# Performance work log

Hardware: AMD Instinct MI355X
Metric: run time of the kernel (lower is better)

The kernel has to match this reference:

```python
import jax, jax.numpy as jnp
import numpy as np

NUM_HEADS = 8
GRAPH_DIM = 64
K_RATIO = 0.1
SIM_THRESH = 0.6


def _gat_layer(h_in, mask, W, a_src, a_dst, b):
    # PyG GATConv (heads=1, eval mode): lin (no bias), alpha = LeakyReLU(a_src.h_j + a_dst.h_i),
    # softmax over source nodes j per target i (edges given by dense mask, self loops included), + bias.
    h = h_in @ W                                   # [N, F]
    asrc = h @ a_src                               # [N] source term
    adst = h @ a_dst                               # [N] target term
    logits = jax.nn.leaky_relu(adst[:, None] + asrc[None, :], 0.2)  # [target i, source j]
    logits = jnp.where(mask.T, logits, -1e30)      # mask[j,i]: edge src j -> dst i (symmetric here)
    alpha = jax.nn.softmax(logits, axis=-1)
    return alpha @ h + b


def _forward(x, w_qkv, w_proj, b_proj, gat0_W, gat0_asrc, gat0_adst, gat0_b,
             gat1_W, gat1_asrc, gat1_adst, gat1_b, w_g2a, b_g2a):
    B, C, H, W = x.shape
    HW = H * W
    nh = NUM_HEADS
    hd = C // nh
    scale = hd ** -0.5
    x_seq = x.reshape(B, C, HW).transpose(0, 2, 1)                 # [B, HW, C]

    # ---- build_spatial_graph ----
    importance = jnp.var(x_seq, axis=-1, ddof=1)                   # torch.var default unbiased
    N = int(HW * K_RATIO)                                          # 102 nodes
    _, top_idx = jax.lax.top_k(importance, N)                      # [B, N]
    feats = jnp.take_along_axis(x_seq, top_idx[..., None], axis=1) # [B, N, C]
    fn = feats / jnp.clip(jnp.linalg.norm(feats, axis=-1, keepdims=True), 1e-12)
    sim = fn @ fn.transpose(0, 2, 1)                               # [B, N, N]
    adj = sim > SIM_THRESH
    adj = adj | jnp.eye(N, dtype=bool)                             # GATConv add_self_loops

    # ---- per-batch GAT stack + graph_to_attn ----
    def per_graph(f, m):
        g = jax.nn.relu(_gat_layer(f, m, gat0_W, gat0_asrc, gat0_adst, gat0_b))
        g = jax.nn.relu(_gat_layer(g, m, gat1_W, gat1_asrc, gat1_adst, gat1_b))
        return jax.nn.sigmoid(g @ w_g2a.T + b_g2a)                 # [N, nh]
    gw = jax.vmap(per_graph)(feats, adj)                           # [B, N, nh]

    # ---- dense multi-head attention ----
    qkv = (x_seq @ w_qkv.T).reshape(B, HW, 3, nh, hd).transpose(2, 0, 3, 1, 4)
    q, k, v = qkv[0], qkv[1], qkv[2]                               # [B, nh, HW, hd]
    scores = jnp.einsum('bhqd,bhkd->bhqk', q, k) * scale           # [B, nh, HW, HW]

    # ---- graph modulation scatter (replaces the nested python loops) ----
    vals = jnp.where(adj[..., None], gw[:, :, None, :] * gw[:, None, :, :], 0.0)  # [B, N, N, nh]
    gm = jnp.zeros_like(scores)
    bidx = jnp.arange(B)[:, None, None]
    gm = gm.at[bidx, :, top_idx[:, :, None], top_idx[:, None, :]].set(vals)
    scores = scores + gm

    attn = jax.nn.softmax(scores, axis=-1)                         # dropout is identity in eval
    out = jnp.einsum('bhqk,bhkd->bhqd', attn, v).transpose(0, 2, 1, 3).reshape(B, HW, C)
    out = out @ w_proj.T + b_proj
    return out.transpose(0, 2, 1).reshape(B, C, H, W)


def setup_inputs() -> dict:
    key = jax.random.key(0)
    ks = jax.random.split(key, 16)
    dim, gd, nh = 256, GRAPH_DIM, NUM_HEADS
    B, H, W = 8, 32, 32
    s = 0.02
    return {
        'x': jax.random.normal(ks[0], (B, dim, H, W), dtype=jnp.float32),
        'w_qkv': s * jax.random.normal(ks[1], (3 * dim, dim), dtype=jnp.float32),
        'w_proj': s * jax.random.normal(ks[2], (dim, dim), dtype=jnp.float32),
        'b_proj': jnp.zeros((dim,), dtype=jnp.float32),
        'gat0_W': s * jax.random.normal(ks[3], (dim, gd), dtype=jnp.float32),
        'gat0_asrc': s * jax.random.normal(ks[4], (gd,), dtype=jnp.float32),
        'gat0_adst': s * jax.random.normal(ks[5], (gd,), dtype=jnp.float32),
        'gat0_b': jnp.zeros((gd,), dtype=jnp.float32),
        'gat1_W': s * jax.random.normal(ks[6], (gd, gd), dtype=jnp.float32),
        'gat1_asrc': s * jax.random.normal(ks[7], (gd,), dtype=jnp.float32),
        'gat1_adst': s * jax.random.normal(ks[8], (gd,), dtype=jnp.float32),
        'gat1_b': jnp.zeros((gd,), dtype=jnp.float32),
        'w_g2a': s * jax.random.normal(ks[9], (nh, gd), dtype=jnp.float32),
        'b_g2a': jnp.zeros((nh,), dtype=jnp.float32),
    }


def reference(x, w_qkv, w_proj, b_proj, gat0_W, gat0_asrc, gat0_adst, gat0_b,
              gat1_W, gat1_asrc, gat1_adst, gat1_b, w_g2a, b_g2a):
    return _forward(x, w_qkv, w_proj, b_proj, gat0_W, gat0_asrc, gat0_adst, gat0_b,
                    gat1_W, gat1_asrc, gat1_adst, gat1_b, w_g2a, b_g2a)
```

## Files before the change

kernel.cpp:

```cpp
#include <hip/hip_runtime.h>
#include <math.h>

#define NB 8
#define CDIM 256
#define HWD 1024
#define NH 8
#define HD 32
#define NN 102
#define GD 64

typedef __attribute__((ext_vector_type(8))) short bf16x8;
typedef __attribute__((ext_vector_type(4))) float f32x4;

__device__ inline short f2bf(float f) {
  union { float f; unsigned u; } v; v.f = f;
  unsigned r = v.u + 0x7fffu + ((v.u >> 16) & 1u);
  return (short)(r >> 16);
}
__device__ inline float bf2f(short s) {
  union { unsigned u; float f; } v;
  v.u = ((unsigned)(unsigned short)s) << 16;
  return v.f;
}

__global__ __launch_bounds__(256) void wsplit_k(const float* __restrict__ w_qkv,
                                                const float* __restrict__ w_proj,
                                                short* __restrict__ wqh, short* __restrict__ wql,
                                                short* __restrict__ wph, short* __restrict__ wpl) {
  int t = blockIdx.x * 256 + threadIdx.x;
  if (t < 196608) {
    float v = w_qkv[t];
    short hi = f2bf(v);
    wqh[t] = hi; wql[t] = f2bf(v - bf2f(hi));
  } else {
    int u = t - 196608;
    float v = w_proj[u];
    short hi = f2bf(v);
    wph[u] = hi; wpl[u] = f2bf(v - bf2f(hi));
  }
}

__global__ __launch_bounds__(256) void xsplit_k(const float* __restrict__ x,
                                                short* __restrict__ xth,
                                                short* __restrict__ xtl) {
  __shared__ float tile[64][65];
  int p0 = blockIdx.x * 64, c0 = blockIdx.y * 64, b = blockIdx.z;
  int t = threadIdx.x;
  {
    int g = t >> 6, p = t & 63;
#pragma unroll
    for (int i = 0; i < 16; ++i) {
      int cc = g * 16 + i;
      tile[cc][p] = x[((size_t)(b * 256 + c0 + cc)) * 1024 + p0 + p];
    }
  }
  __syncthreads();
  {
    int p = t >> 2, cs = (t & 3) * 16;
    size_t rb = ((size_t)(b * 1024 + p0 + p)) * 256 + c0 + cs;
#pragma unroll
    for (int g = 0; g < 4; ++g) {
      short4 hv, lv;
      float f0 = tile[cs + g * 4 + 0][p];
      float f1 = tile[cs + g * 4 + 1][p];
      float f2 = tile[cs + g * 4 + 2][p];
      float f3 = tile[cs + g * 4 + 3][p];
      hv.x = f2bf(f0); lv.x = f2bf(f0 - bf2f(hv.x));
      hv.y = f2bf(f1); lv.y = f2bf(f1 - bf2f(hv.y));
      hv.z = f2bf(f2); lv.z = f2bf(f2 - bf2f(hv.z));
      hv.w = f2bf(f3); lv.w = f2bf(f3 - bf2f(hv.w));
      *(short4*)(xth + rb + g * 4) = hv;
      *(short4*)(xtl + rb + g * 4) = lv;
    }
  }
}

__global__ __launch_bounds__(256) void prep_k(const float* __restrict__ g0W,
                                              const float* __restrict__ g1W,
                                              short* __restrict__ w0bT,
                                              short* __restrict__ w1bT) {
  int t = blockIdx.x * 256 + threadIdx.x;
  if (t < 16384) {
    int c = t >> 6, f = t & 63;
    w0bT[f * 256 + c] = f2bf(g0W[t]);
  } else if (t < 20480) {
    int u2 = t - 16384;
    int c = u2 >> 6, f = u2 & 63;
    w1bT[f * 64 + c] = f2bf(g1W[u2]);
  }
}

__global__ __launch_bounds__(256) void importance_k(const float* __restrict__ x,
                                                    float* __restrict__ imp) {
  __shared__ float red[8][33];
  int bp = blockIdx.x;
  int b = bp >> 5, p0 = (bp & 31) << 5;
  int t = threadIdx.x;
  int pl = t & 31, cg = t >> 5;
  const float* xp = x + (size_t)b * CDIM * HWD + p0 + pl;
  float s = 0.f;
  for (int cc = 0; cc < 32; ++cc) s += xp[(size_t)(cg * 32 + cc) * HWD];
  red[cg][pl] = s;
  __syncthreads();
  float tot = 0.f;
  for (int g = 0; g < 8; ++g) tot += red[g][pl];
  float mean = tot * (1.f / CDIM);
  __syncthreads();
  float v = 0.f;
  for (int cc = 0; cc < 32; ++cc) {
    float d = xp[(size_t)(cg * 32 + cc) * HWD] - mean;
    v += d * d;
  }
  red[cg][pl] = v;
  __syncthreads();
  if (t < 32) {
    float vv = 0.f;
    for (int g = 0; g < 8; ++g) vv += red[g][t];
    imp[b * 1024 + p0 + t] = vv * (1.f / (CDIM - 1));
  }
}

union GraphLDS {
  struct { float sv[1024]; int si[1024]; } tk;
  struct {
    short h0T[64 * 136];
    short alphaB[102 * 136];
    short gB[102 * 72];
  } m;
};

__global__ __launch_bounds__(1024) void graph_k(
    const float* __restrict__ x, const float* __restrict__ imp,
    const short* __restrict__ w0bT, const short* __restrict__ w1bT,
    const float* __restrict__ g0as, const float* __restrict__ g0ad,
    const float* __restrict__ g0b,
    const float* __restrict__ g1as, const float* __restrict__ g1ad,
    const float* __restrict__ g1b,
    const float* __restrict__ wg2a, const float* __restrict__ bg2a,
    int* __restrict__ nodeof, int* __restrict__ topi, short* __restrict__ fnG,
    unsigned char* __restrict__ adjG, float* __restrict__ gwb) {
  __shared__ GraphLDS u;
  __shared__ ushort adjPack[NN][8];
  __shared__ float normL[NN];
  __shared__ float asrcL[NN], adstL[NN];
  __shared__ int topiL[NN];
  int b = blockIdx.x, t = threadIdx.x;
  int wv = t >> 6, lane = t & 63, quad = lane >> 4, l16 = lane & 15;

  u.tk.sv[t] = imp[b * 1024 + t];
  u.tk.si[t] = t;
  nodeof[b * 1024 + t] = -1;
  __syncthreads();
  for (int k = 2; k <= 1024; k <<= 1) {
    for (int j = k >> 1; j > 0; j >>= 1) {
      int ixj = t ^ j;
      if (ixj > t) {
        bool up = ((t & k) == 0);
        float a = u.tk.sv[t], c = u.tk.sv[ixj];
        if ((a > c) == up) {
          u.tk.sv[t] = c; u.tk.sv[ixj] = a;
          int ti = u.tk.si[t]; u.tk.si[t] = u.tk.si[ixj]; u.tk.si[ixj] = ti;
        }
      }
      __syncthreads();
    }
  }
  if (t >= 1024 - NN) {
    int n = 1023 - t;
    int idx = u.tk.si[t];
    topiL[n] = idx;
    topi[b * 128 + n] = idx;
    nodeof[b * 1024 + idx] = n;
  }
  __syncthreads();

  {
    int n = t >> 3, g = t & 7;
    if (n < NN) {
      int idx = topiL[n];
      const float* xb = x + (size_t)b * CDIM * HWD + idx;
      float vbuf[32];
      float ssl = 0.f;
#pragma unroll
      for (int cc = 0; cc < 32; ++cc) {
        float v = xb[(size_t)(g * 32 + cc) * HWD];
        vbuf[cc] = v;
        ssl += v * v;
      }
      ssl += __shfl_xor(ssl, 1);
      ssl += __shfl_xor(ssl, 2);
      ssl += __shfl_xor(ssl, 4);
      float nrm = sqrtf(ssl);
      float rn = 1.f / fmaxf(nrm, 1e-12f);
      if (g == 0) normL[n] = nrm;
      short* fp = fnG + ((size_t)b * 112 + n) * 256 + g * 32;
#pragma unroll
      for (int cc = 0; cc < 32; cc += 4) {
        short4 s4 = {f2bf(vbuf[cc] * rn), f2bf(vbuf[cc + 1] * rn),
                     f2bf(vbuf[cc + 2] * rn), f2bf(vbuf[cc + 3] * rn)};
        *(short4*)(fp + cc) = s4;
      }
    }
  }
  for (int e = t; e < 64 * 34; e += 1024) {
    int f = e / 34, c = 102 + (e % 34);
    u.m.h0T[f * 136 + c] = 0;
  }
  __syncthreads();

  for (int tile = wv; tile < 49; tile += 16) {
    int I = tile / 7, J = tile % 7;
    const short* ap = fnG + ((size_t)b * 112 + I * 16 + l16) * 256 + quad * 8;
    const short* bp = fnG + ((size_t)b * 112 + J * 16 + l16) * 256 + quad * 8;
    f32x4 acc = (f32x4){0.f, 0.f, 0.f, 0.f};
#pragma unroll
    for (int kb = 0; kb < 8; ++kb)
      acc = __builtin_amdgcn_mfma_f32_16x16x32_bf16(*(const bf16x8*)(ap + kb * 32),
                                                    *(const bf16x8*)(bp + kb * 32), acc, 0, 0, 0);
#pragma unroll
    for (int r = 0; r < 4; ++r) {
      int i = I * 16 + quad * 4 + r, j = J * 16 + l16;
      bool e = (acc[r] > 0.6f) || (i == j);
      unsigned long long m = __ballot(e);
      if (l16 == 0) {
        int row = I * 16 + quad * 4 + r;
        if (row < NN) adjPack[row][J] = (ushort)((m >> (quad * 16)) & 0xFFFFull);
      }
      if (i < NN && j < NN) adjG[(size_t)b * NN * NN + i * NN + j] = e ? 1 : 0;
    }
  }
  __syncthreads();

  for (int tile = wv; tile < 28; tile += 16) {
    int mt = tile >> 2, nt = tile & 3;
    const short* ap = fnG + ((size_t)b * 112 + mt * 16 + l16) * 256 + quad * 8;
    const short* bp = w0bT + (nt * 16 + l16) * 256 + quad * 8;
    f32x4 acc = (f32x4){0.f, 0.f, 0.f, 0.f};
#pragma unroll
    for (int kb = 0; kb < 8; ++kb)
      acc = __builtin_amdgcn_mfma_f32_16x16x32_bf16(*(const bf16x8*)(ap + kb * 32),
                                                    *(const bf16x8*)(bp + kb * 32), acc, 0, 0, 0);
    int f = nt * 16 + l16;
#pragma unroll
    for (int r = 0; r < 4; ++r) {
      int node = mt * 16 + quad * 4 + r;
      if (node < NN) u.m.h0T[f * 136 + node] = f2bf(acc[r] * normL[node]);
    }
  }
  __syncthreads();

  for (int layer = 0; layer < 2; ++layer) {
    const float* avs = layer ? g1as : g0as;
    const float* avd = layer ? g1ad : g0ad;
    const float* bias = layer ? g1b : g0b;
    {
      int n = t >> 3, g = t & 7;
      if (n < NN) {
        float s1 = 0.f, s2 = 0.f;
#pragma unroll
        for (int uu = 0; uu < 8; ++uu) {
          int f = g * 8 + uu;
          float hv = bf2f(u.m.h0T[f * 136 + n]);
          s1 += hv * avs[f];
          s2 += hv * avd[f];
        }
        s1 += __shfl_xor(s1, 1); s1 += __shfl_xor(s1, 2); s1 += __shfl_xor(s1, 4);
        s2 += __shfl_xor(s2, 1); s2 += __shfl_xor(s2, 2); s2 += __shfl_xor(s2, 4);
        if (g == 0) { asrcL[n] = s1; adstL[n] = s2; }
      }
    }
    __syncthreads();
    for (int i = wv; i < NN; i += 16) {
      float zi = adstL[i];
      int j1 = 64 + lane;
      bool e0 = (adjPack[i][lane >> 4] >> (lane & 15)) & 1;
      bool e1 = (j1 < NN) && ((adjPack[i][j1 >> 4] >> (j1 & 15)) & 1);
      float p0 = 0.f, p1 = 0.f;
      if (e0) { float z = zi + asrcL[lane]; p0 = __expf(z > 0.f ? z : 0.2f * z); }
      if (e1) { float z = zi + asrcL[j1]; p1 = __expf(z > 0.f ? z : 0.2f * z); }
      float s = p0 + p1;
      s += __shfl_xor(s, 1); s += __shfl_xor(s, 2); s += __shfl_xor(s, 4);
      s += __shfl_xor(s, 8); s += __shfl_xor(s, 16); s += __shfl_xor(s, 32);
      float inv = 1.f / s;
      u.m.alphaB[i * 136 + lane] = f2bf(p0 * inv);
      u.m.alphaB[i * 136 + 64 + lane] = f2bf(p1 * inv);
    }
    __syncthreads();
    for (int tile = wv; tile < 28; tile += 16) {
      int mt = tile >> 2, nt = tile & 3;
      int ar = mt * 16 + l16; if (ar > NN - 1) ar = NN - 1;
      const short* ap = &u.m.alphaB[ar * 136 + quad * 8];
      const short* bp = &u.m.h0T[(nt * 16 + l16) * 136 + quad * 8];
      f32x4 acc = (f32x4){0.f, 0.f, 0.f, 0.f};
#pragma unroll
      for (int kb = 0; kb < 4; ++kb)
        acc = __builtin_amdgcn_mfma_f32_16x16x32_bf16(*(const bf16x8*)(ap + kb * 32),
                                                      *(const bf16x8*)(bp + kb * 32), acc, 0, 0, 0);
      int f = nt * 16 + l16;
      float bv = bias[f];
#pragma unroll
      for (int r = 0; r < 4; ++r) {
        int i = mt * 16 + quad * 4 + r;
        if (i < NN) u.m.gB[i * 72 + f] = f2bf(fmaxf(acc[r] + bv, 0.f));
      }
    }
    __syncthreads();
    if (layer == 0) {
      for (int tile = wv; tile < 28; tile += 16) {
        int mt = tile >> 2, nt = tile & 3;
        int ar = mt * 16 + l16; if (ar > NN - 1) ar = NN - 1;
        const short* ap = &u.m.gB[ar * 72 + quad * 8];
        const short* bp = w1bT + (nt * 16 + l16) * 64 + quad * 8;
        f32x4 acc = (f32x4){0.f, 0.f, 0.f, 0.f};
#pragma unroll
        for (int kb = 0; kb < 2; ++kb)
          acc = __builtin_amdgcn_mfma_f32_16x16x32_bf16(*(const bf16x8*)(ap + kb * 32),
                                                        *(const bf16x8*)(bp + kb * 32), acc, 0, 0, 0);
        int f = nt * 16 + l16;
#pragma unroll
        for (int r = 0; r < 4; ++r) {
          int node = mt * 16 + quad * 4 + r;
          if (node < NN) u.m.h0T[f * 136 + node] = f2bf(acc[r]);
        }
      }
      __syncthreads();
    }
  }
  float* wgL = (float*)&u.m.alphaB[0];
  if (t < 512) wgL[t] = wg2a[t];
  __syncthreads();
  if (t < NN * NH) {
    int n = t >> 3, h = t & 7;
    float z = bg2a[h];
#pragma unroll
    for (int c = 0; c < GD; ++c) z += bf2f(u.m.gB[n * 72 + c]) * wgL[h * 64 + c];
    gwb[((size_t)b * NN + n) * NH + h] = 1.f / (1.f + __expf(-z));
  }
}

__global__ __launch_bounds__(128) void posadj_k(const int* __restrict__ nodeof,
                                                const int* __restrict__ topi,
                                                const unsigned char* __restrict__ adjG,
                                                const float* __restrict__ gwb,
                                                unsigned long long* __restrict__ posadj,
                                                float* __restrict__ gwp) {
  int b = blockIdx.y, p = blockIdx.x * 128 + threadIdx.x;
  int n = nodeof[b * 1024 + p];
#pragma unroll
  for (int h = 0; h < 8; ++h)
    gwp[(size_t)(b * 8 + h) * 1024 + p] =
        (n >= 0) ? gwb[((size_t)b * NN + n) * NH + h] : 0.f;
  unsigned long long m[16];
#pragma unroll
  for (int w = 0; w < 16; ++w) m[w] = 0;
  if (n >= 0) {
    const unsigned char* ar = adjG + (size_t)b * NN * NN + (size_t)n * NN;
    for (int nj = 0; nj < NN; ++nj) {
      if (ar[nj]) {
        int pj = topi[b * 128 + nj];
        m[pj >> 6] |= 1ull << (pj & 63);
      }
    }
  }
  unsigned long long* dst = posadj + (size_t)(b * 1024 + p) * 16;
#pragma unroll
  for (int w = 0; w < 16; ++w) dst[w] = m[w];
}

__global__ __launch_bounds__(256, 4) void qkv_k(const short* __restrict__ xth,
                                                const short* __restrict__ xtl,
                                                const short* __restrict__ wqh,
                                                const short* __restrict__ wql,
                                                short* __restrict__ qhp, short* __restrict__ qlp,
                                                short* __restrict__ khp, short* __restrict__ klp,
                                                short* __restrict__ vtp) {
  __shared__ short vs_s[4][32 * 24];
  int t = threadIdx.x, wid = t >> 6, lane = t & 63, quad = lane >> 4, l16 = lane & 15;
  int m0 = blockIdx.x * 64, y = blockIdx.y;
  int b = m0 >> 10;
  int row = m0 + wid * 16 + l16;
  int p_base = (m0 & 1023) + wid * 16;
  int qi = y >> 3, n0 = (y & 7) * 32;
  const short* wh = wqh + ((size_t)qi * 256 + n0) * 256;
  const short* wl = wql + ((size_t)qi * 256 + n0) * 256;
  const short* arh = xth + (size_t)row * 256 + quad * 8;
  const short* arl = xtl + (size_t)row * 256 + quad * 8;
  f32x4 acc[2];
  acc[0] = (f32x4){0.f, 0.f, 0.f, 0.f};
  acc[1] = (f32x4){0.f, 0.f, 0.f, 0.f};
#pragma unroll
  for (int kb = 0; kb < 8; ++kb) {
    bf16x8 ah = *(const bf16x8*)(arh + kb * 32);
    bf16x8 al = *(const bf16x8*)(arl + kb * 32);
#pragma unroll
    for (int nt = 0; nt < 2; ++nt) {
      size_t wo = (size_t)(nt * 16 + l16) * 256 + kb * 32 + quad * 8;
      bf16x8 bh_ = *(const bf16x8*)(wh + wo);
      bf16x8 bl_ = *(const bf16x8*)(wl + wo);
      acc[nt] = __builtin_amdgcn_mfma_f32_16x16x32_bf16(ah, bh_, acc[nt], 0, 0, 0);
      acc[nt] = __builtin_amdgcn_mfma_f32_16x16x32_bf16(ah, bl_, acc[nt], 0, 0, 0);
      acc[nt] = __builtin_amdgcn_mfma_f32_16x16x32_bf16(al, bh_, acc[nt], 0, 0, 0);
    }
  }
  if (qi < 2) {
    const float scale = (qi == 0) ? 0.17677669529663687f : 1.f;
    short* hp = (qi == 0) ? qhp : khp;
    short* lp = (qi == 0) ? qlp : klp;
#pragma unroll
    for (int nt = 0; nt < 2; ++nt) {
      int nq = n0 + nt * 16 + l16;
      int h = nq >> 5, d = nq & 31;
#pragma unroll
      for (int r = 0; r < 4; ++r) {
        int p = p_base + quad * 4 + r;
        float v = acc[nt][r] * scale;
        short hi = f2bf(v);
        short lo = f2bf(v - bf2f(hi));
        size_t e = ((size_t)(b * 8 + h) * 1024 + p) * 32 + d;
        hp[e] = hi;
        lp[e] = lo;
      }
    }
  } else {
    short* vs = &vs_s[wid][0];
#pragma unroll
    for (int nt = 0; nt < 2; ++nt)
#pragma unroll
      for (int r = 0; r < 4; ++r)
        vs[(nt * 16 + l16) * 24 + quad * 4 + r] = f2bf(acc[nt][r]);
    int cl = lane >> 1, hf = lane & 1;
    int nq = n0 + cl;
    int h = nq >> 5, d = nq & 31;
    size_t rb = ((size_t)(b * 8 + h) * 32 + d) * 1024 + p_base + hf * 8;
    *(bf16x8*)(vtp + rb) = *(const bf16x8*)(vs + cl * 24 + hf * 8);
  }
}

__global__ __launch_bounds__(256, 4) void attn_k(const short* __restrict__ qh,
                                                 const short* __restrict__ ql,
                                                 const short* __restrict__ kh,
                                                 const short* __restrict__ kl,
                                                 const short* __restrict__ vt,
                                                 const float* __restrict__ gwp,
                                                 const unsigned long long* __restrict__ posadj,
                                                 float* __restrict__ po,
                                                 float* __restrict__ pl) {
  __shared__ __align__(16) short p_s[4][16 * 72];
  __shared__ float aw_s[4][16];
  int t = threadIdx.x;
  int wid = t >> 6, lane = t & 63, quad = lane >> 4, l16 = lane & 15;
  int bh = blockIdx.x, b = bh >> 3;
  int qt = blockIdx.y, khalf = blockIdx.z;
  int q0 = qt * 64 + wid * 16;
  size_t base = (size_t)bh * 32768;
  short* pw = &p_s[wid][0];
  float* aw = &aw_s[wid][0];

  size_t qoff = base + (size_t)(q0 + l16) * 32 + quad * 8;
  bf16x8 qhf = *(const bf16x8*)(qh + qoff);
  bf16x8 qlf = *(const bf16x8*)(ql + qoff);

  const float* gwpBH = gwp + (size_t)bh * 1024;
  const unsigned long long* paB = posadj + (size_t)b * 1024 * 16;
  float grq[4];
#pragma unroll
  for (int r = 0; r < 4; ++r) grq[r] = gwpBH[q0 + quad * 4 + r];

  f32x4 ot[2];
  ot[0] = (f32x4){0.f, 0.f, 0.f, 0.f};
  ot[1] = (f32x4){0.f, 0.f, 0.f, 0.f};
  float l_r[4] = {0.f, 0.f, 0.f, 0.f};

  for (int ch = khalf * 8; ch < khalf * 8 + 8; ++ch) {
    int c0 = ch * 64;
    bf16x8 khf[4], klf[4];
#pragma unroll
    for (int ni = 0; ni < 4; ++ni) {
      size_t off = base + (size_t)(c0 + ni * 16 + l16) * 32 + quad * 8;
      khf[ni] = *(const bf16x8*)(kh + off);
      klf[ni] = *(const bf16x8*)(kl + off);
    }
    bf16x8 vaf[2][2];
#pragma unroll
    for (int mi = 0; mi < 2; ++mi)
#pragma unroll
      for (int ks = 0; ks < 2; ++ks)
        vaf[mi][ks] = *(const bf16x8*)(vt + base + (size_t)(mi * 16 + l16) * 1024 +
                                       c0 + ks * 32 + quad * 8);
    float gc[4];
#pragma unroll
    for (int ni = 0; ni < 4; ++ni) gc[ni] = gwpBH[c0 + ni * 16 + l16];
    unsigned long long mr[4];
#pragma unroll
    for (int r = 0; r < 4; ++r)
      mr[r] = paB[(size_t)(q0 + quad * 4 + r) * 16 + ch];
    f32x4 s[4];
#pragma unroll
    for (int ni = 0; ni < 4; ++ni) {
      f32x4 a = (f32x4){0.f, 0.f, 0.f, 0.f};
      a = __builtin_amdgcn_mfma_f32_16x16x32_bf16(qhf, khf[ni], a, 0, 0, 0);
      a = __builtin_amdgcn_mfma_f32_16x16x32_bf16(qhf, klf[ni], a, 0, 0, 0);
      a = __builtin_amdgcn_mfma_f32_16x16x32_bf16(qlf, khf[ni], a, 0, 0, 0);
      s[ni] = a;
    }
#pragma unroll
    for (int r = 0; r < 4; ++r) {
#pragma unroll
      for (int ni = 0; ni < 4; ++ni) {
        bool bit = (mr[r] >> (ni * 16 + l16)) & 1ull;
        s[ni][r] += bit ? grq[r] * gc[ni] : 0.f;
      }
    }
#pragma unroll
    for (int r = 0; r < 4; ++r) {
      float e0 = __expf(s[0][r]);
      float e1 = __expf(s[1][r]);
      float e2 = __expf(s[2][r]);
      float e3 = __expf(s[3][r]);
      l_r[r] += (e0 + e1) + (e2 + e3);
      int prow = (quad * 4 + r) * 72;
      pw[prow + 0 + l16] = f2bf(e0);
      pw[prow + 16 + l16] = f2bf(e1);
      pw[prow + 32 + l16] = f2bf(e2);
      pw[prow + 48 + l16] = f2bf(e3);
    }
#pragma unroll
    for (int ks = 0; ks < 2; ++ks) {
      bf16x8 pb = *(const bf16x8*)(pw + l16 * 72 + ks * 32 + quad * 8);
      ot[0] = __builtin_amdgcn_mfma_f32_16x16x32_bf16(vaf[0][ks], pb, ot[0], 0, 0, 0);
      ot[1] = __builtin_amdgcn_mfma_f32_16x16x32_bf16(vaf[1][ks], pb, ot[1], 0, 0, 0);
    }
  }
#pragma unroll
  for (int r = 0; r < 4; ++r) {
    float ls = l_r[r];
    ls += __shfl_xor(ls, 1);
    ls += __shfl_xor(ls, 2);
    ls += __shfl_xor(ls, 4);
    ls += __shfl_xor(ls, 8);
    if (l16 == 0) aw[quad * 4 + r] = ls;
  }
  float* os = (float*)pw;
#pragma unroll
  for (int mi = 0; mi < 2; ++mi)
#pragma unroll
    for (int r = 0; r < 4; ++r)
      os[l16 * 36 + mi * 16 + quad * 4 + r] = ot[mi][r];
  int bht = bh * 16 + qt;
  size_t pob = (((size_t)bht * 2 + khalf) * 64 + wid * 16) * 32;
  int qr2 = lane >> 2, dg = (lane & 3) * 8;
  *(float4*)&po[pob + qr2 * 32 + dg] = *(float4*)&os[qr2 * 36 + dg];
  *(float4*)&po[pob + qr2 * 32 + dg + 4] = *(float4*)&os[qr2 * 36 + dg + 4];
  if (lane < 16) pl[((size_t)bht * 2 + khalf) * 64 + wid * 16 + lane] = aw[lane];
}

__global__ __launch_bounds__(256) void reduce_k(const float* __restrict__ po,
                                                const float* __restrict__ pl,
                                                short* __restrict__ aoh,
                                                short* __restrict__ aol) {
  int bht = blockIdx.x;
  int bh = bht >> 4, qt = bht & 15;
  int b = bh >> 3, h = bh & 7;
  int t = threadIdx.x;
  int q = t >> 2, dg = (t & 3) * 8;
  size_t b0 = (((size_t)bht * 2 + 0) * 64 + q) * 32 + dg;
  size_t b1 = (((size_t)bht * 2 + 1) * 64 + q) * 32 + dg;
  float4 a0 = *(const float4*)&po[b0];
  float4 a1 = *(const float4*)&po[b0 + 4];
  float4 c0 = *(const float4*)&po[b1];
  float4 c1 = *(const float4*)&po[b1 + 4];
  float l = pl[((size_t)bht * 2) * 64 + q] + pl[((size_t)bht * 2 + 1) * 64 + q];
  float inv = 1.f / l;
  float f[8] = {(a0.x + c0.x) * inv, (a0.y + c0.y) * inv,
                (a0.z + c0.z) * inv, (a0.w + c0.w) * inv,
                (a1.x + c1.x) * inv, (a1.y + c1.y) * inv,
                (a1.z + c1.z) * inv, (a1.w + c1.w) * inv};
  bf16x8 hv, lv;
#pragma unroll
  for (int j = 0; j < 8; ++j) {
    hv[j] = f2bf(f[j]);
    lv[j] = f2bf(f[j] - bf2f(hv[j]));
  }
  size_t ob = (size_t)(b * 1024 + qt * 64 + q) * 256 + h * 32 + dg;
  *(bf16x8*)(aoh + ob) = hv;
  *(bf16x8*)(aol + ob) = lv;
}

__global__ __launch_bounds__(256, 4) void proj_k(const short* __restrict__ aoh,
                                                 const short* __restrict__ aol,
                                                 const short* __restrict__ wph,
                                                 const short* __restrict__ wpl,
                                                 const float* __restrict__ bias,
                                                 float* __restrict__ out) {
  __shared__ float os_s[4][32 * 20];
  int t = threadIdx.x, wid = t >> 6, lane = t & 63, quad = lane >> 4, l16 = lane & 15;
  int m0 = blockIdx.x * 64, n0 = blockIdx.y * 32;
  int b = m0 >> 10;
  int row = m0 + wid * 16 + l16;
  int p_base = (m0 & 1023) + wid * 16;
  const short* arh = aoh + (size_t)row * 256 + quad * 8;
  const short* arl = aol + (size_t)row * 256 + quad * 8;
  f32x4 acc[2];
  acc[0] = (f32x4){0.f, 0.f, 0.f, 0.f};
  acc[1] = (f32x4){0.f, 0.f, 0.f, 0.f};
#pragma unroll
  for (int kb = 0; kb < 8; ++kb) {
// ... 27 lines not shown
extern "C" void kernel_launch(void* const* d_in, const int* in_sizes, int n_in,
                              void* d_out, int out_size, void* d_ws, size_t ws_size,
                              hipStream_t stream) {
  const float* x      = (const float*)d_in[0];
  const float* w_qkv  = (const float*)d_in[1];
  const float* w_proj = (const float*)d_in[2];
  const float* b_proj = (const float*)d_in[3];
  const float* g0W    = (const float*)d_in[4];
  const float* g0as   = (const float*)d_in[5];
  const float* g0ad   = (const float*)d_in[6];
  const float* g0b    = (const float*)d_in[7];
  const float* g1W    = (const float*)d_in[8];
  const float* g1as   = (const float*)d_in[9];
  const float* g1ad   = (const float*)d_in[10];
  const float* g1b    = (const float*)d_in[11];
  const float* wg2a   = (const float*)d_in[12];
  const float* bg2a   = (const float*)d_in[13];
  float* out = (float*)d_out;
  float* ws = (float*)d_ws;

  size_t o = 0;
  auto alloc = [&](size_t nf) { float* p = ws + o; o += (nf + 15) & ~(size_t)15; return p; };
  float* imp    = alloc(8 * 1024);
  int*   nodeof = (int*)alloc(8 * 1024);
  int*   topi   = (int*)alloc(8 * 128);
  short* fnG    = (short*)alloc(8 * 112 * 256 / 2);
  short* w0bT   = (short*)alloc(256 * 64 / 2);
  short* w1bT   = (short*)alloc(64 * 64 / 2);
  unsigned char* adj = (unsigned char*)alloc((8 * NN * NN + 3) / 4 + 16);
  float* gwb    = alloc(8 * NN * 8);
  unsigned long long* posadj = (unsigned long long*)alloc(8 * 1024 * 16 * 2);
  float* gwp    = alloc(64 * 1024);
  short* xth    = (short*)alloc(1048576);
  short* xtl    = (short*)alloc(1048576);
  short* wqh    = (short*)alloc(98304);
  short* wql    = (short*)alloc(98304);
  short* wph    = (short*)alloc(32768);
  short* wpl    = (short*)alloc(32768);
  short* qh     = (short*)alloc(1048576);
  short* ql     = (short*)alloc(1048576);
  short* kh     = (short*)alloc(1048576);
  short* kl     = (short*)alloc(1048576);
  short* vt     = (short*)alloc(1048576);
  short* aoh    = (short*)alloc(1048576);
  short* aol    = (short*)alloc(1048576);
  float* po     = alloc((size_t)1024 * 2 * 64 * 32);
  float* plv    = alloc((size_t)1024 * 2 * 64);
  if (ws_size < o * sizeof(float)) return;

  importance_k<<<256, 256, 0, stream>>>(x, imp);
  wsplit_k<<<1024, 256, 0, stream>>>(w_qkv, w_proj, wqh, wql, wph, wpl);
  xsplit_k<<<dim3(16, 4, 8), 256, 0, stream>>>(x, xth, xtl);
  prep_k<<<80, 256, 0, stream>>>(g0W, g1W, w0bT, w1bT);
  graph_k<<<8, 1024, 0, stream>>>(x, imp, w0bT, w1bT, g0as, g0ad, g0b,
                                  g1as, g1ad, g1b, wg2a, bg2a,
                                  nodeof, topi, fnG, adj, gwb);
  posadj_k<<<dim3(8, 8), 128, 0, stream>>>(nodeof, topi, adj, gwb, posadj, gwp);
  qkv_k<<<dim3(128, 24), 256, 0, stream>>>(xth, xtl, wqh, wql, qh, ql, kh, kl, vt);
  attn_k<<<dim3(64, 16, 2), 256, 0, stream>>>(qh, ql, kh, kl, vt, gwp, posadj, po, plv);
  reduce_k<<<1024, 256, 0, stream>>>(po, plv, aoh, aol);
  proj_k<<<dim3(128, 8), 256, 0, stream>>>(aoh, aol, wph, wpl, b_proj, out);
}
```

Measured before the change: 365.8 us.

## Fuse prep, posadj and split-K reduce kernels; restructure graph and attention stages

Merges the GAT weight prep into the weight-split kernel, folds posadj construction into graph_k using LDS adjacency bits, and removes the attention split-K plus reduce kernel by having each attention block process all 16 key chunks and normalize in place. graph_k now reads pre-split bf16 transposed x instead of strided fp32 x, applies the norm scaling after the similarity MFMA, and computes the attention-logit dot products inside the linear-layer MFMA epilogue. The posadj layout is transposed to chunk-major, and the qkv store paths are restaged through LDS for wider writes. This cuts kernel launches and intermediate global traffic, but the attention grid is halved (1024 blocks instead of 2048), which lowers parallelism, and graph_k still runs on only 8 blocks.

Result: faster. 300.9 us (-17.7%).

```diff
diff --git a/kernel.cpp b/kernel.cpp
--- a/kernel.cpp
+++ b/kernel.cpp
@@ -23,20 +23,37 @@
   return v.f;
 }
 
-__global__ __launch_bounds__(256) void wsplit_k(const float* __restrict__ w_qkv,
-                                                const float* __restrict__ w_proj,
-                                                short* __restrict__ wqh, short* __restrict__ wql,
-                                                short* __restrict__ wph, short* __restrict__ wpl) {
-  int t = blockIdx.x * 256 + threadIdx.x;
-  if (t < 196608) {
-    float v = w_qkv[t];
-    short hi = f2bf(v);
-    wqh[t] = hi; wql[t] = f2bf(v - bf2f(hi));
+__global__ __launch_bounds__(256) void wsplitprep_k(const float* __restrict__ w_qkv,
+                                                    const float* __restrict__ w_proj,
+                                                    const float* __restrict__ g0W,
+                                                    const float* __restrict__ g1W,
+                                                    short* __restrict__ wqh, short* __restrict__ wql,
+                                                    short* __restrict__ wph, short* __restrict__ wpl,
+                                                    short* __restrict__ w0bT,
+                                                    short* __restrict__ w1bT) {
+  int bx = blockIdx.x;
+  if (bx < 1024) {
+    int t = bx * 256 + threadIdx.x;
+    if (t < 196608) {
+      float v = w_qkv[t];
+      short hi = f2bf(v);
+      wqh[t] = hi; wql[t] = f2bf(v - bf2f(hi));
+    } else {
+      int u = t - 196608;
+      float v = w_proj[u];
+      short hi = f2bf(v);
+      wph[u] = hi; wpl[u] = f2bf(v - bf2f(hi));
+    }
   } else {
-    int u = t - 196608;
-    float v = w_proj[u];
-    short hi = f2bf(v);
-    wph[u] = hi; wpl[u] = f2bf(v - bf2f(hi));
+    int t = (bx - 1024) * 256 + threadIdx.x;
+    if (t < 16384) {
+      int c = t >> 6, f = t & 63;
+      w0bT[f * 256 + c] = f2bf(g0W[t]);
+    } else if (t < 20480) {
+      int u2 = t - 16384;
+      int c = u2 >> 6, f = u2 & 63;
+      w1bT[f * 64 + c] = f2bf(g1W[u2]);
+    }
   }
 }
 
@@ -75,21 +92,6 @@
   }
 }
 
-__global__ __launch_bounds__(256) void prep_k(const float* __restrict__ g0W,
-                                              const float* __restrict__ g1W,
-                                              short* __restrict__ w0bT,
-                                              short* __restrict__ w1bT) {
-  int t = blockIdx.x * 256 + threadIdx.x;
-  if (t < 16384) {
-    int c = t >> 6, f = t & 63;
-    w0bT[f * 256 + c] = f2bf(g0W[t]);
-  } else if (t < 20480) {
-    int u2 = t - 16384;
-    int c = u2 >> 6, f = u2 & 63;
-    w1bT[f * 64 + c] = f2bf(g1W[u2]);
-  }
-}
-
 __global__ __launch_bounds__(256) void importance_k(const float* __restrict__ x,
                                                     float* __restrict__ imp) {
   __shared__ float red[8][33];
@@ -122,34 +124,37 @@
 
 union GraphLDS {
   struct { float sv[1024]; int si[1024]; } tk;
-  struct {
-    short h0T[64 * 136];
-    short alphaB[102 * 136];
-    short gB[102 * 72];
-  } m;
+  short featsB[NN * 264];
+  struct { short alphaB[NN * 136]; short gB[NN * 72]; } ly;
 };
 
 __global__ __launch_bounds__(1024) void graph_k(
-    const float* __restrict__ x, const float* __restrict__ imp,
+    const float* __restrict__ imp,
+    const short* __restrict__ xth, const short* __restrict__ xtl,
     const short* __restrict__ w0bT, const short* __restrict__ w1bT,
     const float* __restrict__ g0as, const float* __restrict__ g0ad,
     const float* __restrict__ g0b,
     const float* __restrict__ g1as, const float* __restrict__ g1ad,
     const float* __restrict__ g1b,
     const float* __restrict__ wg2a, const float* __restrict__ bg2a,
-    int* __restrict__ nodeof, int* __restrict__ topi, short* __restrict__ fnG,
-    unsigned char* __restrict__ adjG, float* __restrict__ gwb) {
+    short* __restrict__ h0tG,
+    float* __restrict__ gwp,
+    unsigned long long* __restrict__ posadj)
+{
   __shared__ GraphLDS u;
   __shared__ ushort adjPack[NN][8];
-  __shared__ float normL[NN];
-  __shared__ float asrcL[NN], adstL[NN];
+  __shared__ float rnL[NN];
+  __shared__ float asrcL[112], adstL[112];
   __shared__ int topiL[NN];
+  __shared__ int nodeofL[1024];
   int b = blockIdx.x, t = threadIdx.x;
   int wv = t >> 6, lane = t & 63, quad = lane >> 4, l16 = lane & 15;
+  short* hb = h0tG + (size_t)b * 64 * 128;
 
   u.tk.sv[t] = imp[b * 1024 + t];
   u.tk.si[t] = t;
-  nodeof[b * 1024 + t] = -1;
+  nodeofL[t] = -1;
+  for (int e = t; e < 64 * 26; e += 1024) hb[(e / 26) * 128 + 102 + (e % 26)] = 0;
   __syncthreads();
   for (int k = 2; k <= 1024; k <<= 1) {
     for (int j = k >> 1; j > 0; j >>= 1) {
@@ -169,49 +174,42 @@
     int n = 1023 - t;
     int idx = u.tk.si[t];
     topiL[n] = idx;
-    topi[b * 128 + n] = idx;
-    nodeof[b * 1024 + idx] = n;
+    nodeofL[idx] = n;
   }
   __syncthreads();
 
   {
     int n = t >> 3, g = t & 7;
     if (n < NN) {
-      int idx = topiL[n];
-      const float* xb = x + (size_t)b * CDIM * HWD + idx;
-      float vbuf[32];
-      float ssl = 0.f;
-#pragma unroll
-      for (int cc = 0; cc < 32; ++cc) {
-        float v = xb[(size_t)(g * 32 + cc) * HWD];
-        vbuf[cc] = v;
-        ssl += v * v;
-      }
-      ssl += __shfl_xor(ssl, 1);
-      ssl += __shfl_xor(ssl, 2);
-      ssl += __shfl_xor(ssl, 4);
-      float nrm = sqrtf(ssl);
-      float rn = 1.f / fmaxf(nrm, 1e-12f);
-      if (g == 0) normL[n] = nrm;
-      short* fp = fnG + ((size_t)b * 112 + n) * 256 + g * 32;
-#pragma unroll
-      for (int cc = 0; cc < 32; cc += 4) {
-        short4 s4 = {f2bf(vbuf[cc] * rn), f2bf(vbuf[cc + 1] * rn),
-                     f2bf(vbuf[cc + 2] * rn), f2bf(vbuf[cc + 3] * rn)};
-        *(short4*)(fp + cc) = s4;
-      }
-    }
-  }
-  for (int e = t; e < 64 * 34; e += 1024) {
-    int f = e / 34, c = 102 + (e % 34);
-    u.m.h0T[f * 136 + c] = 0;
+      int p = topiL[n];
+      const short* xh = xth + ((size_t)(b * 1024 + p)) * 256 + g * 32;
+      const short* xl = xtl + ((size_t)(b * 1024 + p)) * 256 + g * 32;
+      float ss = 0.f;
+#pragma unroll
+      for (int c8 = 0; c8 < 4; ++c8) {
+        bf16x8 hv = *(const bf16x8*)(xh + c8 * 8);
+        bf16x8 lv = *(const bf16x8*)(xl + c8 * 8);
+#pragma unroll
+        for (int j = 0; j < 8; ++j) {
+          float f = bf2f(hv[j]) + bf2f(lv[j]);
+          ss += f * f;
+        }
+        *(bf16x8*)(&u.featsB[n * 264 + g * 32 + c8 * 8]) = hv;
+      }
+      ss += __shfl_xor(ss, 1);
+      ss += __shfl_xor(ss, 2);
+      ss += __shfl_xor(ss, 4);
+      if (g == 0) rnL[n] = 1.f / fmaxf(sqrtf(ss), 1e-12f);
+    }
   }
   __syncthreads();
 
   for (int tile = wv; tile < 49; tile += 16) {
     int I = tile / 7, J = tile % 7;
-    const short* ap = fnG + ((size_t)b * 112 + I * 16 + l16) * 256 + quad * 8;
-    const short* bp = fnG + ((size_t)b * 112 + J * 16 + l16) * 256 + quad * 8;
+    int rA = I * 16 + l16; if (rA > NN - 1) rA = NN - 1;
+    int rB = J * 16 + l16; if (rB > NN - 1) rB = NN - 1;
+    const short* ap = &u.featsB[rA * 264 + quad * 8];
+    const short* bp = &u.featsB[rB * 264 + quad * 8];
     f32x4 acc = (f32x4){0.f, 0.f, 0.f, 0.f};
 #pragma unroll
     for (int kb = 0; kb < 8; ++kb)
@@ -220,56 +218,51 @@
 #pragma unroll
     for (int r = 0; r < 4; ++r) {
       int i = I * 16 + quad * 4 + r, j = J * 16 + l16;
-      bool e = (acc[r] > 0.6f) || (i == j);
+      bool e = (i < NN && j < NN) &&
+               ((acc[r] * rnL[i < NN ? i : 0] * rnL[j < NN ? j : 0] > 0.6f) || (i == j));
       unsigned long long m = __ballot(e);
-      if (l16 == 0) {
-        int row = I * 16 + quad * 4 + r;
-        if (row < NN) adjPack[row][J] = (ushort)((m >> (quad * 16)) & 0xFFFFull);
-      }
-      if (i < NN && j < NN) adjG[(size_t)b * NN * NN + i * NN + j] = e ? 1 : 0;
-    }
-  }
-  __syncthreads();
-
-  for (int tile = wv; tile < 28; tile += 16) {
-    int mt = tile >> 2, nt = tile & 3;
-    const short* ap = fnG + ((size_t)b * 112 + mt * 16 + l16) * 256 + quad * 8;
-    const short* bp = w0bT + (nt * 16 + l16) * 256 + quad * 8;
-    f32x4 acc = (f32x4){0.f, 0.f, 0.f, 0.f};
-#pragma unroll
-    for (int kb = 0; kb < 8; ++kb)
-      acc = __builtin_amdgcn_mfma_f32_16x16x32_bf16(*(const bf16x8*)(ap + kb * 32),
-                                                    *(const bf16x8*)(bp + kb * 32), acc, 0, 0, 0);
-    int f = nt * 16 + l16;
+      if (l16 == 0 && i < NN) adjPack[i][J] = (ushort)((m >> (quad * 16)) & 0xFFFFull);
+    }
+  }
+  __syncthreads();
+
+  if (wv < 7) {
+    int mt = wv;
+    int ar = mt * 16 + l16; if (ar > NN - 1) ar = NN - 1;
+    const short* ap = &u.featsB[ar * 264 + quad * 8];
+    float s1[4] = {0.f, 0.f, 0.f, 0.f}, s2[4] = {0.f, 0.f, 0.f, 0.f};
+#pragma unroll
+    for (int nt = 0; nt < 4; ++nt) {
+      const short* bp = w0bT + (nt * 16 + l16) * 256 + quad * 8;
+      f32x4 acc = (f32x4){0.f, 0.f, 0.f, 0.f};
+#pragma unroll
+      for (int kb = 0; kb < 8; ++kb)
+        acc = __builtin_amdgcn_mfma_f32_16x16x32_bf16(*(const bf16x8*)(ap + kb * 32),
+                                                      *(const bf16x8*)(bp + kb * 32), acc, 0, 0, 0);
+      int f = nt * 16 + l16;
+      float a_s = g0as[f], a_d = g0ad[f];
+#pragma unroll
+      for (int r = 0; r < 4; ++r) {
+        int node = mt * 16 + quad * 4 + r;
+        if (node < NN) hb[f * 128 + node] = f2bf(acc[r]);
+        s1[r] += acc[r] * a_s;
+        s2[r] += acc[r] * a_d;
+      }
+    }
 #pragma unroll
     for (int r = 0; r < 4; ++r) {
+      float v1 = s1[r], v2 = s2[r];
+      v1 += __shfl_xor(v1, 1); v1 += __shfl_xor(v1, 2);
+      v1 += __shfl_xor(v1, 4); v1 += __shfl_xor(v1, 8);
+      v2 += __shfl_xor(v2, 1); v2 += __shfl_xor(v2, 2);
+      v2 += __shfl_xor(v2, 4); v2 += __shfl_xor(v2, 8);
       int node = mt * 16 + quad * 4 + r;
-      if (node < NN) u.m.h0T[f * 136 + node] = f2bf(acc[r] * normL[node]);
+      if (l16 == 0 && node < NN) { asrcL[node] = v1; adstL[node] = v2; }
     }
   }
   __syncthreads();
 
   for (int layer = 0; layer < 2; ++layer) {
-    const float* avs = layer ? g1as : g0as;
-    const float* avd = layer ? g1ad : g0ad;
-    const float* bias = layer ? g1b : g0b;
-    {
-      int n = t >> 3, g = t & 7;
-      if (n < NN) {
-        float s1 = 0.f, s2 = 0.f;
-#pragma unroll
-        for (int uu = 0; uu < 8; ++uu) {
-          int f = g * 8 + uu;
-          float hv = bf2f(u.m.h0T[f * 136 + n]);
-          s1 += hv * avs[f];
-          s2 += hv * avd[f];
-        }
-        s1 += __shfl_xor(s1, 1); s1 += __shfl_xor(s1, 2); s1 += __shfl_xor(s1, 4);
-        s2 += __shfl_xor(s2, 1); s2 += __shfl_xor(s2, 2); s2 += __shfl_xor(s2, 4);
-        if (g == 0) { asrcL[n] = s1; adstL[n] = s2; }
-      }
-    }
-    __syncthreads();
     for (int i = wv; i < NN; i += 16) {
       float zi = adstL[i];
       int j1 = 64 + lane;
@@ -282,89 +275,108 @@
       s += __shfl_xor(s, 1); s += __shfl_xor(s, 2); s += __shfl_xor(s, 4);
       s += __shfl_xor(s, 8); s += __shfl_xor(s, 16); s += __shfl_xor(s, 32);
       float inv = 1.f / s;
-      u.m.alphaB[i * 136 + lane] = f2bf(p0 * inv);
-      u.m.alphaB[i * 136 + 64 + lane] = f2bf(p1 * inv);
+      u.ly.alphaB[i * 136 + lane] = f2bf(p0 * inv);
+      u.ly.alphaB[i * 136 + 64 + lane] = f2bf(p1 * inv);
     }
     __syncthreads();
-    for (int tile = wv; tile < 28; tile += 16) {
-      int mt = tile >> 2, nt = tile & 3;
-      int ar = mt * 16 + l16; if (ar > NN - 1) ar = NN - 1;
-      const short* ap = &u.m.alphaB[ar * 136 + quad * 8];
-      const short* bp = &u.m.h0T[(nt * 16 + l16) * 136 + quad * 8];
-      f32x4 acc = (f32x4){0.f, 0.f, 0.f, 0.f};
-#pragma unroll
-      for (int kb = 0; kb < 4; ++kb)
-        acc = __builtin_amdgcn_mfma_f32_16x16x32_bf16(*(const bf16x8*)(ap + kb * 32),
-                                                      *(const bf16x8*)(bp + kb * 32), acc, 0, 0, 0);
-      int f = nt * 16 + l16;
-      float bv = bias[f];
-#pragma unroll
-      for (int r = 0; r < 4; ++r) {
-        int i = mt * 16 + quad * 4 + r;
-        if (i < NN) u.m.gB[i * 72 + f] = f2bf(fmaxf(acc[r] + bv, 0.f));
-      }
-    }
-    __syncthreads();
-    if (layer == 0) {
+    {
+      const float* bias = layer ? g1b : g0b;
       for (int tile = wv; tile < 28; tile += 16) {
         int mt = tile >> 2, nt = tile & 3;
         int ar = mt * 16 + l16; if (ar > NN - 1) ar = NN - 1;
-        const short* ap = &u.m.gB[ar * 72 + quad * 8];
-        const short* bp = w1bT + (nt * 16 + l16) * 64 + quad * 8;
+        const short* ap = &u.ly.alphaB[ar * 136 + quad * 8];
+        const short* bp = hb + (nt * 16 + l16) * 128 + quad * 8;
         f32x4 acc = (f32x4){0.f, 0.f, 0.f, 0.f};
 #pragma unroll
-        for (int kb = 0; kb < 2; ++kb)
+        for (int kb = 0; kb < 4; ++kb)
           acc = __builtin_amdgcn_mfma_f32_16x16x32_bf16(*(const bf16x8*)(ap + kb * 32),
                                                         *(const bf16x8*)(bp + kb * 32), acc, 0, 0, 0);
         int f = nt * 16 + l16;
+        float bv = bias[f];
 #pragma unroll
         for (int r = 0; r < 4; ++r) {
+          int i = mt * 16 + quad * 4 + r;
+          if (i < NN) u.ly.gB[i * 72 + f] = f2bf(fmaxf(acc[r] + bv, 0.f));
+        }
+      }
+    }
+    __syncthreads();
+    if (layer == 0) {
+      if (wv < 7) {
+        int mt = wv;
+        int ar = mt * 16 + l16; if (ar > NN - 1) ar = NN - 1;
+        const short* ap = &u.ly.gB[ar * 72 + quad * 8];
+        float s1[4] = {0.f, 0.f, 0.f, 0.f}, s2[4] = {0.f, 0.f, 0.f, 0.f};
+#pragma unroll
+        for (int nt = 0; nt < 4; ++nt) {
+          const short* bp = w1bT + (nt * 16 + l16) * 64 + quad * 8;
+          f32x4 acc = (f32x4){0.f, 0.f, 0.f, 0.f};
+#pragma unroll
+          for (int kb = 0; kb < 2; ++kb)
+            acc = __builtin_amdgcn_mfma_f32_16x16x32_bf16(*(const bf16x8*)(ap + kb * 32),
+                                                          *(const bf16x8*)(bp + kb * 32), acc, 0, 0, 0);
+          int f = nt * 16 + l16;
+          float a_s = g1as[f], a_d = g1ad[f];
+#pragma unroll
+          for (int r = 0; r < 4; ++r) {
+            int node = mt * 16 + quad * 4 + r;
+            if (node < NN) hb[f * 128 + node] = f2bf(acc[r]);
+            s1[r] += acc[r] * a_s;
+            s2[r] += acc[r] * a_d;
+          }
+        }
+#pragma unroll
+        for (int r = 0; r < 4; ++r) {
+          float v1 = s1[r], v2 = s2[r];
+          v1 += __shfl_xor(v1, 1); v1 += __shfl_xor(v1, 2);
+          v1 += __shfl_xor(v1, 4); v1 += __shfl_xor(v1, 8);
+          v2 += __shfl_xor(v2, 1); v2 += __shfl_xor(v2, 2);
+          v2 += __shfl_xor(v2, 4); v2 += __shfl_xor(v2, 8);
           int node = mt * 16 + quad * 4 + r;
-          if (node < NN) u.m.h0T[f * 136 + node] = f2bf(acc[r]);
+          if (l16 == 0 && node < NN) { asrcL[node] = v1; adstL[node] = v2; }
         }
       }
       __syncthreads();
     }
   }
-  float* wgL = (float*)&u.m.alphaB[0];
+
+  float* wgL = (float*)&u.ly.alphaB[0];
+  float* gwN = wgL + 512;
   if (t < 512) wgL[t] = wg2a[t];
   __syncthreads();
   if (t < NN * NH) {
     int n = t >> 3, h = t & 7;
     float z = bg2a[h];
 #pragma unroll
-    for (int c = 0; c < GD; ++c) z += bf2f(u.m.gB[n * 72 + c]) * wgL[h * 64 + c];
-    gwb[((size_t)b * NN + n) * NH + h] = 1.f / (1.f + __expf(-z));
-  }
-}
-
-__global__ __launch_bounds__(128) void posadj_k(const int* __restrict__ nodeof,
-                                                const int* __restrict__ topi,
-                                                const unsigned char* __restrict__ adjG,
-                                                const float* __restrict__ gwb,
-                                                unsigned long long* __restrict__ posadj,
-                                                float* __restrict__ gwp) {
-  int b = blockIdx.y, p = blockIdx.x * 128 + threadIdx.x;
-  int n = nodeof[b * 1024 + p];
-#pragma unroll
-  for (int h = 0; h < 8; ++h)
-    gwp[(size_t)(b * 8 + h) * 1024 + p] =
-        (n >= 0) ? gwb[((size_t)b * NN + n) * NH + h] : 0.f;
-  unsigned long long m[16];
-#pragma unroll
-  for (int w = 0; w < 16; ++w) m[w] = 0;
-  if (n >= 0) {
-    const unsigned char* ar = adjG + (size_t)b * NN * NN + (size_t)n * NN;
-    for (int nj = 0; nj < NN; ++nj) {
-      if (ar[nj]) {
-        int pj = topi[b * 128 + nj];
-        m[pj >> 6] |= 1ull << (pj & 63);
-      }
-    }
-  }
-  unsigned long long* dst = posadj + (size_t)(b * 1024 + p) * 16;
-#pragma unroll
-  for (int w = 0; w < 16; ++w) dst[w] = m[w];
+    for (int c = 0; c < GD; ++c) z += bf2f(u.ly.gB[n * 72 + c]) * wgL[h * 64 + c];
+    gwN[n * 8 + h] = 1.f / (1.f + __expf(-z));
+  }
+  __syncthreads();
+
+  {
+    int p = t;
+    int n = nodeofL[p];
+#pragma unroll
+    for (int h = 0; h < 8; ++h)
+      gwp[(size_t)(b * 8 + h) * 1024 + p] = (n >= 0) ? gwN[n * 8 + h] : 0.f;
+    unsigned long long m[16];
+#pragma unroll
+    for (int w = 0; w < 16; ++w) m[w] = 0;
+    if (n >= 0) {
+      for (int w = 0; w < 7; ++w) {
+        unsigned bits = adjPack[n][w];
+        while (bits) {
+          int j = __ffs(bits) - 1;
+          int pj = topiL[w * 16 + j];
+          m[pj >> 6] |= 1ull << (pj & 63);
+          bits &= bits - 1;
+        }
+      }
+    }
+#pragma unroll
+    for (int w = 0; w < 16; ++w)
+      posadj[((size_t)b * 16 + w) * 1024 + p] = m[w];
+  }
 }
 
 __global__ __launch_bounds__(256, 4) void qkv_k(const short* __restrict__ xth,
@@ -374,7 +386,7 @@
                                                 short* __restrict__ qhp, short* __restrict__ qlp,
                                                 short* __restrict__ khp, short* __restrict__ klp,
                                                 short* __restrict__ vtp) {
-  __shared__ short vs_s[4][32 * 24];
+  __shared__ short st_s[4][16 * 40 * 2];
   int t = threadIdx.x, wid = t >> 6, lane = t & 63, quad = lane >> 4, l16 = lane & 15;
   int m0 = blockIdx.x * 64, y = blockIdx.y;
   int b = m0 >> 10;
@@ -402,37 +414,41 @@
       acc[nt] = __builtin_amdgcn_mfma_f32_16x16x32_bf16(al, bh_, acc[nt], 0, 0, 0);
     }
   }
+  int h = n0 >> 5;
   if (qi < 2) {
     const float scale = (qi == 0) ? 0.17677669529663687f : 1.f;
     short* hp = (qi == 0) ? qhp : khp;
     short* lp = (qi == 0) ? qlp : klp;
+    short* vsh = &st_s[wid][0];
+    short* vsl = &st_s[wid][640];
 #pragma unroll
     for (int nt = 0; nt < 2; ++nt) {
-      int nq = n0 + nt * 16 + l16;
-      int h = nq >> 5, d = nq & 31;
+      int d = nt * 16 + l16;
 #pragma unroll
       for (int r = 0; r < 4; ++r) {
-        int p = p_base + quad * 4 + r;
         float v = acc[nt][r] * scale;
         short hi = f2bf(v);
-        short lo = f2bf(v - bf2f(hi));
-        size_t e = ((size_t)(b * 8 + h) * 1024 + p) * 32 + d;
-        hp[e] = hi;
-        lp[e] = lo;
-      }
-    }
+        vsh[(quad * 4 + r) * 40 + d] = hi;
+        vsl[(quad * 4 + r) * 40 + d] = f2bf(v - bf2f(hi));
+      }
+    }
+    int orow = lane >> 2, seg = lane & 3;
+    size_t e = ((size_t)(b * 8 + h) * 1024 + p_base + orow) * 32 + seg * 8;
+    *(bf16x8*)(hp + e) = *(const bf16x8*)(vsh + orow * 40 + seg * 8);
+    *(bf16x8*)(lp + e) = *(const bf16x8*)(vsl + orow * 40 + seg * 8);
   } else {
-    short* vs = &vs_s[wid][0];
-#pragma unroll
-    for (int nt = 0; nt < 2; ++nt)
+    short* vsv = &st_s[0][0];
+#pragma unroll
+    for (int nt = 0; nt < 2; ++nt) {
+      int d = nt * 16 + l16;
 #pragma unroll
       for (int r = 0; r < 4; ++r)
-        vs[(nt * 16 + l16) * 24 + quad * 4 + r] = f2bf(acc[nt][r]);
-    int cl = lane >> 1, hf = lane & 1;
-    int nq = n0 + cl;
-    int h = nq >> 5, d = nq & 31;
-    size_t rb = ((size_t)(b * 8 + h) * 32 + d) * 1024 + p_base + hf * 8;
-    *(bf16x8*)(vtp + rb) = *(const bf16x8*)(vs + cl * 24 + hf * 8);
+        vsv[d * 72 + (quad * 4 + r) * 4 + wid] = f2bf(acc[nt][r]);
+    }
+    __syncthreads();
+    int d = t >> 3, g = t & 7;
+    size_t rb = ((size_t)(b * 8 + h) * 32 + d) * 1024 + (m0 & 1023) + g * 8;
+    *(bf16x8*)(vtp + rb) = *(const bf16x8*)(vsv + d * 72 + g * 8);
   }
 }
 
@@ -443,15 +459,14 @@
                                                  const short* __restrict__ vt,
                                                  const float* __restrict__ gwp,
                                                  const unsigned long long* __restrict__ posadj,
-                                                 float* __restrict__ po,
-                                                 float* __restrict__ pl) {
+                                                 short* __restrict__ aoh,
+                                                 short* __restrict__ aol) {
   __shared__ __align__(16) short p_s[4][16 * 72];
   __shared__ float aw_s[4][16];
   int t = threadIdx.x;
   int wid = t >> 6, lane = t & 63, quad = lane >> 4, l16 = lane & 15;
-  int bh = blockIdx.x, b = bh >> 3;
-  int qt = blockIdx.y, khalf = blockIdx.z;
-  int q0 = qt * 64 + wid * 16;
+  int bh = blockIdx.x, b = bh >> 3, h = bh & 7;
+  int q0 = blockIdx.y * 64 + wid * 16;
   size_t base = (size_t)bh * 32768;
   short* pw = &p_s[wid][0];
   float* aw = &aw_s[wid][0];
@@ -461,7 +476,7 @@
   bf16x8 qlf = *(const bf16x8*)(ql + qoff);
 
   const float* gwpBH = gwp + (size_t)bh * 1024;
-  const unsigned long long* paB = posadj + (size_t)b * 1024 * 16;
+  const unsigned long long* paB = posadj + (size_t)b * 16 * 1024;
   float grq[4];
 #pragma unroll
   for (int r = 0; r < 4; ++r) grq[r] = gwpBH[q0 + quad * 4 + r];
@@ -471,7 +486,7 @@
   ot[1] = (f32x4){0.f, 0.f, 0.f, 0.f};
   float l_r[4] = {0.f, 0.f, 0.f, 0.f};
 
-  for (int ch = khalf * 8; ch < khalf * 8 + 8; ++ch) {
+  for (int ch = 0; ch < 16; ++ch) {
     int c0 = ch * 64;
     bf16x8 khf[4], klf[4];
 #pragma unroll
@@ -493,7 +508,7 @@
     unsigned long long mr[4];
 #pragma unroll
     for (int r = 0; r < 4; ++r)
-      mr[r] = paB[(size_t)(q0 + quad * 4 + r) * 16 + ch];
+      mr[r] = paB[(size_t)ch * 1024 + q0 + quad * 4 + r];
     f32x4 s[4];
 #pragma unroll
     for (int ni = 0; ni < 4; ++ni) {
@@ -518,11 +533,8 @@
       float e2 = __expf(s[2][r]);
       float e3 = __expf(s[3][r]);
       l_r[r] += (e0 + e1) + (e2 + e3);
-      int prow = (quad * 4 + r) * 72;
-      pw[prow + 0 + l16] = f2bf(e0);
-      pw[prow + 16 + l16] = f2bf(e1);
-      pw[prow + 32 + l16] = f2bf(e2);
-      pw[prow + 48 + l16] = f2bf(e3);
+      short4 pq = {f2bf(e0), f2bf(e1), f2bf(e2), f2bf(e3)};
+      *(short4*)(pw + (quad * 4 + r) * 72 + l16 * 4) = pq;
     }
 #pragma unroll
     for (int ks = 0; ks < 2; ++ks) {
@@ -538,50 +550,28 @@
     ls += __shfl_xor(ls, 2);
     ls += __shfl_xor(ls, 4);
     ls += __shfl_xor(ls, 8);
-    if (l16 == 0) aw[quad * 4 + r] = ls;
-  }
+    if (l16 == 0) aw[quad * 4 + r] = 1.f / ls;
+  }
+  float li = aw[l16];
+  ot[0] *= li;
+  ot[1] *= li;
   float* os = (float*)pw;
 #pragma unroll
   for (int mi = 0; mi < 2; ++mi)
 #pragma unroll
     for (int r = 0; r < 4; ++r)
       os[l16 * 36 + mi * 16 + quad * 4 + r] = ot[mi][r];
-  int bht = bh * 16 + qt;
-  size_t pob = (((size_t)bht * 2 + khalf) * 64 + wid * 16) * 32;
   int qr2 = lane >> 2, dg = (lane & 3) * 8;
-  *(float4*)&po[pob + qr2 * 32 + dg] = *(float4*)&os[qr2 * 36 + dg];
-  *(float4*)&po[pob + qr2 * 32 + dg + 4] = *(float4*)&os[qr2 * 36 + dg + 4];
-  if (lane < 16) pl[((size_t)bht * 2 + khalf) * 64 + wid * 16 + lane] = aw[lane];
-}
-
-__global__ __launch_bounds__(256) void reduce_k(const float* __restrict__ po,
-                                                const float* __restrict__ pl,
-                                                short* __restrict__ aoh,
-                                                short* __restrict__ aol) {
-  int bht = blockIdx.x;
-  int bh = bht >> 4, qt = bht & 15;
-  int b = bh >> 3, h = bh & 7;
-  int t = threadIdx.x;
-  int q = t >> 2, dg = (t & 3) * 8;
-  size_t b0 = (((size_t)bht * 2 + 0) * 64 + q) * 32 + dg;
-  size_t b1 = (((size_t)bht * 2 + 1) * 64 + q) * 32 + dg;
-  float4 a0 = *(const float4*)&po[b0];
-  float4 a1 = *(const float4*)&po[b0 + 4];
-  float4 c0 = *(const float4*)&po[b1];
-  float4 c1 = *(const float4*)&po[b1 + 4];
-  float l = pl[((size_t)bht * 2) * 64 + q] + pl[((size_t)bht * 2 + 1) * 64 + q];
-  float inv = 1.f / l;
-  float f[8] = {(a0.x + c0.x) * inv, (a0.y + c0.y) * inv,
-                (a0.z + c0.z) * inv, (a0.w + c0.w) * inv,
-                (a1.x + c1.x) * inv, (a1.y + c1.y) * inv,
-                (a1.z + c1.z) * inv, (a1.w + c1.w) * inv};
+  float f[8];
+  *(float4*)&f[0] = *(float4*)&os[qr2 * 36 + dg];
+  *(float4*)&f[4] = *(float4*)&os[qr2 * 36 + dg + 4];
   bf16x8 hv, lv;
 #pragma unroll
   for (int j = 0; j < 8; ++j) {
     hv[j] = f2bf(f[j]);
     lv[j] = f2bf(f[j] - bf2f(hv[j]));
   }
-  size_t ob = (size_t)(b * 1024 + qt * 64 + q) * 256 + h * 32 + dg;
+  size_t ob = (size_t)(b * 1024 + q0 + qr2) * 256 + h * 32 + dg;
   *(bf16x8*)(aoh + ob) = hv;
   *(bf16x8*)(aol + ob) = lv;
 }
@@ -655,15 +645,11 @@
   size_t o = 0;
   auto alloc = [&](size_t nf) { float* p = ws + o; o += (nf + 15) & ~(size_t)15; return p; };
   float* imp    = alloc(8 * 1024);
-  int*   nodeof = (int*)alloc(8 * 1024);
-  int*   topi   = (int*)alloc(8 * 128);
-  short* fnG    = (short*)alloc(8 * 112 * 256 / 2);
   short* w0bT   = (short*)alloc(256 * 64 / 2);
   short* w1bT   = (short*)alloc(64 * 64 / 2);
-  unsigned char* adj = (unsigned char*)alloc((8 * NN * NN + 3) / 4 + 16);
-  float* gwb    = alloc(8 * NN * 8);
-  unsigned long long* posadj = (unsigned long long*)alloc(8 * 1024 * 16 * 2);
+  short* h0tG   = (short*)alloc(8 * 64 * 128 / 2);
   float* gwp    = alloc(64 * 1024);
+  unsigned long long* posadj = (unsigned long long*)alloc(8 * 16 * 1024 * 2);
   short* xth    = (short*)alloc(1048576);
   short* xtl    = (short*)alloc(1048576);
   short* wqh    = (short*)alloc(98304);
@@ -677,20 +663,16 @@
   short* vt     = (short*)alloc(1048576);
   short* aoh    = (short*)alloc(1048576);
   short* aol    = (short*)alloc(1048576);
-  float* po     = alloc((size_t)1024 * 2 * 64 * 32);
-  float* plv    = alloc((size_t)1024 * 2 * 64);
   if (ws_size < o * sizeof(float)) return;
 
   importance_k<<<256, 256, 0, stream>>>(x, imp);
-  wsplit_k<<<1024, 256, 0, stream>>>(w_qkv, w_proj, wqh, wql, wph, wpl);
+  wsplitprep_k<<<1104, 256, 0, stream>>>(w_qkv, w_proj, g0W, g1W,
+                                         wqh, wql, wph, wpl, w0bT, w1bT);
   xsplit_k<<<dim3(16, 4, 8), 256, 0, stream>>>(x, xth, xtl);
-  prep_k<<<80, 256, 0, stream>>>(g0W, g1W, w0bT, w1bT);
-  graph_k<<<8, 1024, 0, stream>>>(x, imp, w0bT, w1bT, g0as, g0ad, g0b,
-                                  g1as, g1ad, g1b, wg2a, bg2a,
-                                  nodeof, topi, fnG, adj, gwb);
-  posadj_k<<<dim3(8, 8), 128, 0, stream>>>(nodeof, topi, adj, gwb, posadj, gwp);
+  graph_k<<<8, 1024, 0, stream>>>(imp, xth, xtl, w0bT, w1bT,
+                                  g0as, g0ad, g0b, g1as, g1ad, g1b,
+                                  wg2a, bg2a, h0tG, gwp, posadj);
   qkv_k<<<dim3(128, 24), 256, 0, stream>>>(xth, xtl, wqh, wql, qh, ql, kh, kl, vt);
-  attn_k<<<dim3(64, 16, 2), 256, 0, stream>>>(qh, ql, kh, kl, vt, gwp, posadj, po, plv);
-  reduce_k<<<1024, 256, 0, stream>>>(po, plv, aoh, aol);
+  attn_k<<<dim3(64, 16), 256, 0, stream>>>(qh, ql, kh, kl, vt, gwp, posadj, aoh, aol);
   proj_k<<<dim3(128, 8), 256, 0, stream>>>(aoh, aol, wph, wpl, b_proj, out);
 }
```
